# Kernel optimization log

Measured on AMD Instinct MI355X. Metric: run time of the kernel, lower is better.

Reference implementation:

```python
import jax, jax.numpy as jnp
import numpy as np

SAMPLING_FACTOR = 4

def setup_inputs() -> dict:
    key = jax.random.key(0)
    x = jax.random.normal(key, (8, 8192, 512), dtype=jnp.float32)
    return {"x": x}

def reference(x) -> jnp.ndarray:
    # Causal 'avg' pooling: output[i] = mean(x[:, :(i+1)*sf, :]) over time axis.
    # O(L) rewrite of the original O(L^2) loop: prefix cumsum + strided gather.
    B, L, D = x.shape
    sf = SAMPLING_FACTOR
    out_len = L // sf
    csum = jnp.cumsum(x, axis=1)                       # (B, L, D) prefix sums
    idx = jnp.arange(1, out_len + 1) * sf - 1          # end positions (i+1)*sf - 1
    gathered = csum[:, idx, :]                          # (B, out_len, D)
    counts = (idx + 1).astype(x.dtype)[None, :, None]   # window lengths
    return gathered / counts
```

## Files before the change

kernel.cpp:

```cpp
#include <hip/hip_runtime.h>


#define BB   8
#define LL   8192
#define DD4  128
#define NC   128
#define CL   (LL / NC)
#define OL   (LL / 4)

__global__ __launch_bounds__(256) void ds_phase1(const float4* __restrict__ x,
                                                 float4* __restrict__ sums) {
    int tid = blockIdx.x * blockDim.x + threadIdx.x;
    int d4 = tid & (DD4 - 1);
    int c  = (tid >> 7) & (NC - 1);
    int b  = tid >> 14;

    const float4* p = x + ((b * LL + c * CL) * DD4 + d4);
    float sx = 0.f, sy = 0.f, sz = 0.f, sw = 0.f;
    #pragma unroll 8
    for (int j = 0; j < CL; ++j) {
        float4 v = p[j * DD4];
        sx += v.x; sy += v.y; sz += v.z; sw += v.w;
    }
    sums[(b * NC + c) * DD4 + d4] = make_float4(sx, sy, sz, sw);
}

__global__ __launch_bounds__(256) void ds_phase2(const float4* __restrict__ x,
                                                 const float4* __restrict__ sums,
                                                 float4* __restrict__ out) {
    int tid = blockIdx.x * blockDim.x + threadIdx.x;
    int d4 = tid & (DD4 - 1);
    int c  = (tid >> 7) & (NC - 1);
    int b  = tid >> 14;

    float rx = 0.f, ry = 0.f, rz = 0.f, rw = 0.f;
    const float4* sp = sums + b * NC * DD4 + d4;
    #pragma unroll 4
    for (int c2 = 0; c2 < c; ++c2) {
        float4 v = sp[c2 * DD4];
        rx += v.x; ry += v.y; rz += v.z; rw += v.w;
    }

    const float4* p = x + ((b * LL + c * CL) * DD4 + d4);
    float4* o = out + ((b * OL + c * (CL / 4)) * DD4 + d4);
    int base = c * CL;

    #pragma unroll 4
    for (int j = 0; j < CL; j += 4) {
        float4 v0 = p[(j + 0) * DD4];
        float4 v1 = p[(j + 1) * DD4];
        float4 v2 = p[(j + 2) * DD4];
        float4 v3 = p[(j + 3) * DD4];
        rx += v0.x + v1.x + v2.x + v3.x;
        ry += v0.y + v1.y + v2.y + v3.y;
        rz += v0.z + v1.z + v2.z + v3.z;
        rw += v0.w + v1.w + v2.w + v3.w;
        float inv = 1.0f / (float)(base + j + 4);
        o[(j >> 2) * DD4] = make_float4(rx * inv, ry * inv, rz * inv, rw * inv);
    }
}

extern "C" void kernel_launch(void* const* d_in, const int* in_sizes, int n_in,
                              void* d_out, int out_size, void* d_ws, size_t ws_size,
                              hipStream_t stream) {
    const float4* x = (const float4*)d_in[0];
    float4* out = (float4*)d_out;
    float4* sums = (float4*)d_ws;

    const int total = BB * NC * DD4;
    const int block = 256;
    const int grid  = total / block;

    ds_phase1<<<grid, block, 0, stream>>>(x, sums);
    ds_phase2<<<grid, block, 0, stream>>>(x, sums, out);
}
```

Measured before the change: 220.8 us.

## Write local prefix outputs in phase1 and fix them up in phase2

```diff
diff --git a/kernel.cpp b/kernel.cpp
--- a/kernel.cpp
+++ b/kernel.cpp
@@ -6,28 +6,38 @@
 #define DD4  128
 #define NC   128
 #define CL   (LL / NC)
+#define OPC  (CL / 4)
 #define OL   (LL / 4)
 
 __global__ __launch_bounds__(256) void ds_phase1(const float4* __restrict__ x,
-                                                 float4* __restrict__ sums) {
+                                                 float4* __restrict__ sums,
+                                                 float4* __restrict__ out) {
     int tid = blockIdx.x * blockDim.x + threadIdx.x;
     int d4 = tid & (DD4 - 1);
     int c  = (tid >> 7) & (NC - 1);
     int b  = tid >> 14;
 
-    const float4* p = x + ((b * LL + c * CL) * DD4 + d4);
+    const float4* p = x + (((size_t)b * LL + c * CL) * DD4 + d4);
+    float4* o = out + (((size_t)b * OL + c * OPC) * DD4 + d4);
+
     float sx = 0.f, sy = 0.f, sz = 0.f, sw = 0.f;
-    #pragma unroll 8
-    for (int j = 0; j < CL; ++j) {
-        float4 v = p[j * DD4];
-        sx += v.x; sy += v.y; sz += v.z; sw += v.w;
+    #pragma unroll 4
+    for (int j = 0; j < CL; j += 4) {
+        float4 v0 = p[(j + 0) * DD4];
+        float4 v1 = p[(j + 1) * DD4];
+        float4 v2 = p[(j + 2) * DD4];
+        float4 v3 = p[(j + 3) * DD4];
+        sx += v0.x + v1.x + v2.x + v3.x;
+        sy += v0.y + v1.y + v2.y + v3.y;
+        sz += v0.z + v1.z + v2.z + v3.z;
+        sw += v0.w + v1.w + v2.w + v3.w;
+        o[(j >> 2) * DD4] = make_float4(sx, sy, sz, sw);
     }
     sums[(b * NC + c) * DD4 + d4] = make_float4(sx, sy, sz, sw);
 }
 
-__global__ __launch_bounds__(256) void ds_phase2(const float4* __restrict__ x,
-                                                 const float4* __restrict__ sums,
-                                                 float4* __restrict__ out) {
+__global__ __launch_bounds__(256) void ds_phase2(float4* __restrict__ out,
+                                                 const float4* __restrict__ sums) {
     int tid = blockIdx.x * blockDim.x + threadIdx.x;
     int d4 = tid & (DD4 - 1);
     int c  = (tid >> 7) & (NC - 1);
@@ -36,27 +46,24 @@
     float rx = 0.f, ry = 0.f, rz = 0.f, rw = 0.f;
     const float4* sp = sums + b * NC * DD4 + d4;
     #pragma unroll 4
-    for (int c2 = 0; c2 < c; ++c2) {
-        float4 v = sp[c2 * DD4];
+    for (int q = 0; q < c; ++q) {
+        float4 v = sp[q * DD4];
         rx += v.x; ry += v.y; rz += v.z; rw += v.w;
     }
 
-    const float4* p = x + ((b * LL + c * CL) * DD4 + d4);
-    float4* o = out + ((b * OL + c * (CL / 4)) * DD4 + d4);
-    int base = c * CL;
+    float4* o = out + (((size_t)b * OL + c * OPC) * DD4 + d4);
+    const int base = c * CL;
 
-    #pragma unroll 4
-    for (int j = 0; j < CL; j += 4) {
-        float4 v0 = p[(j + 0) * DD4];
-        float4 v1 = p[(j + 1) * DD4];
-        float4 v2 = p[(j + 2) * DD4];
-        float4 v3 = p[(j + 3) * DD4];
-        rx += v0.x + v1.x + v2.x + v3.x;
-        ry += v0.y + v1.y + v2.y + v3.y;
-        rz += v0.z + v1.z + v2.z + v3.z;
-        rw += v0.w + v1.w + v2.w + v3.w;
-        float inv = 1.0f / (float)(base + j + 4);
-        o[(j >> 2) * DD4] = make_float4(rx * inv, ry * inv, rz * inv, rw * inv);
+    float4 v[OPC];
+    #pragma unroll
+    for (int k = 0; k < OPC; ++k) v[k] = o[(size_t)k * DD4];
+    #pragma unroll
+    for (int k = 0; k < OPC; ++k) {
+        const float inv = 1.0f / (float)(base + 4 * k + 4);
+        o[(size_t)k * DD4] = make_float4((v[k].x + rx) * inv,
+                                         (v[k].y + ry) * inv,
+                                         (v[k].z + rz) * inv,
+                                         (v[k].w + rw) * inv);
     }
 }
 
@@ -71,6 +78,6 @@
     const int block = 256;
     const int grid  = total / block;
 
-    ds_phase1<<<grid, block, 0, stream>>>(x, sums);
-    ds_phase2<<<grid, block, 0, stream>>>(x, sums, out);
+    ds_phase1<<<grid, block, 0, stream>>>(x, sums, out);
+    ds_phase2<<<grid, block, 0, stream>>>(out, sums);
 }
```

Measured after the change: 213.9 us. -3.1%, faster.
